# Optimization experiments

Hardware: AMD Instinct MI355X
Metric: run time of the kernel (lower is better)

## Reference

```python
import jax, jax.numpy as jnp
import numpy as np

B, S, D, H = 16, 512, 128, 8  # batch, seq, input_size, num_heads
DH = D * H


def setup_inputs() -> dict:
    key = jax.random.key(0)
    ks = jax.random.split(key, 10)
    s_in = 1.0 / np.sqrt(D)
    s_out = 1.0 / np.sqrt(DH)
    return {
        "input1": jax.random.normal(ks[0], (B, S, D), dtype=jnp.float32),
        "input2": jax.random.normal(ks[1], (B, S, D), dtype=jnp.float32),
        "Wq": jax.random.normal(ks[2], (D, DH), dtype=jnp.float32) * s_in,
        "bq": jax.random.normal(ks[3], (DH,), dtype=jnp.float32) * 0.01,
        "Wk": jax.random.normal(ks[4], (D, DH), dtype=jnp.float32) * s_in,
        "bk": jax.random.normal(ks[5], (DH,), dtype=jnp.float32) * 0.01,
        "Wv": jax.random.normal(ks[6], (D, DH), dtype=jnp.float32) * s_in,
        "bv": jax.random.normal(ks[7], (DH,), dtype=jnp.float32) * 0.01,
        "Wo": jax.random.normal(ks[8], (DH, DH), dtype=jnp.float32) * s_out,
        "bo": jax.random.normal(ks[9], (DH,), dtype=jnp.float32) * 0.01,
    }


def reference(input1, input2, Wq, bq, Wk, bk, Wv, bv, Wo, bo):
    b = input1.shape[0]
    d, dh = Wq.shape
    h = dh // d
    scale = 1.0 / (d ** 0.5)

    def proj(x, W, bias):
        # faithful to torch: view(B, h, -1, d) on a [B, S, h*d] tensor (row-major)
        return (x @ W + bias).reshape(b, h, -1, d)

    def half(xq, xk, xv):
        q = proj(xq, Wq, bq)  # [B,h,S,d]
        k = proj(xk, Wk, bk)
        v = proj(xv, Wv, bv)
        scores = jnp.einsum('bhqd,bhkd->bhqk', q, k) * scale
        attn = jax.nn.softmax(scores, axis=-1)
        # original transposes attention before the value matmul: attn^T @ v
        out = jnp.einsum('bhqk,bhqd->bhkd', attn, v)
        out = out.reshape(b, -1, h * d)
        return out @ Wo + bo

    out1 = half(input1, input2, input1)
    out2 = half(input2, input1, input2)
    return (out1, out2)
```

## Files before the change

kernel.cpp:

```cpp
#include <hip/hip_runtime.h>
#include <cstdint>
#include <cstddef>

using f32x4 = __attribute__((ext_vector_type(4))) float;
using s16x8 = __attribute__((ext_vector_type(8))) short;
typedef uint16_t u16;
typedef uint32_t u32;

__device__ __forceinline__ u16 f2bf(float x) {
  union { float f; u32 u; } v; v.f = x;
  u32 r = v.u + 0x7FFFu + ((v.u >> 16) & 1u);
  return (u16)(r >> 16);
}

__device__ __forceinline__ void async16(void* ldsdst, const void* gsrc) {
  __builtin_amdgcn_global_load_lds(
      (const __attribute__((address_space(1))) u32*)gsrc,
      (__attribute__((address_space(3))) u32*)ldsdst, 16, 0, 0);
}

__global__ void cast_x(const float* __restrict__ in1, const float* __restrict__ in2,
                       u16* __restrict__ X) {
  int i = blockIdx.x * blockDim.x + threadIdx.x;
  const float* src = (i < 262144) ? (in1 + (size_t)i * 4) : (in2 + (size_t)(i - 262144) * 4);
  float4 v = *(const float4*)src;
  u16 o0 = f2bf(v.x), o1 = f2bf(v.y), o2 = f2bf(v.z), o3 = f2bf(v.w);
  u32 w0 = (u32)o0 | ((u32)o1 << 16);
  u32 w1 = (u32)o2 | ((u32)o3 << 16);
  *(uint2*)(X + (size_t)i * 4) = make_uint2(w0, w1);
}

__global__ void transp_w(const float* __restrict__ W, u16* __restrict__ Wt, int R, int C) {
  __shared__ float tile[32][33];
  int bx = blockIdx.x * 32;
  int by = blockIdx.y * 32;
  int tx = threadIdx.x, ty = threadIdx.y;
  #pragma unroll
  for (int i = 0; i < 4; ++i)
    tile[ty + i * 8][tx] = W[(size_t)(by + ty + i * 8) * C + bx + tx];
  __syncthreads();
  #pragma unroll
  for (int i = 0; i < 4; ++i)
    Wt[(size_t)(bx + ty + i * 8) * R + by + tx] = f2bf(tile[tx][ty + i * 8]);
}

template<int KDIM, bool OUTBF16>
__global__ __launch_bounds__(256, 2) void gemm16(
    const u16* __restrict__ A, const u16* __restrict__ Bt,
    const float* __restrict__ bias, void* __restrict__ outp) {
  __shared__ char lds[32768];
  char* Asw = lds;
  char* Bsw = lds + 16384;
  const int t = threadIdx.x;
  const int w = t >> 6, l = t & 63;
  const int l15 = l & 15, lg = l >> 4;
  const int wm = w >> 1, wn = w & 1;
  const size_t m0 = (size_t)blockIdx.x * 128;
  const int n0 = blockIdx.y * 128;

  f32x4 acc[4][4] = {};

  for (int k0 = 0; k0 < KDIM; k0 += 64) {
    #pragma unroll
    for (int p = 0; p < 4; ++p) {
      int idx = p * 256 + t;
      int row = idx >> 3, u = idx & 7;
      const char* sa = (const char*)(A + (m0 + row) * (size_t)KDIM + k0) + ((u ^ (row & 7)) << 4);
      async16(Asw + p * 4096 + w * 1024, sa);
      const char* sb = (const char*)(Bt + (size_t)(n0 + row) * KDIM + k0) + ((u ^ (row & 7)) << 4);
      async16(Bsw + p * 4096 + w * 1024, sb);
    }
    __syncthreads();
    s16x8 af[4][2], bfr[4][2];
    #pragma unroll
    for (int it = 0; it < 4; ++it) {
      int m = wm * 64 + it * 16 + l15;
      int n = wn * 64 + it * 16 + l15;
      #pragma unroll
      for (int st = 0; st < 2; ++st) {
        af[it][st]  = *(const s16x8*)(Asw + m * 128 + ((lg * 16 + st * 64) ^ ((m & 7) << 4)));
        bfr[it][st] = *(const s16x8*)(Bsw + n * 128 + ((lg * 16 + st * 64) ^ ((n & 7) << 4)));
      }
    }
    #pragma unroll
    for (int st = 0; st < 2; ++st)
      #pragma unroll
      for (int mt = 0; mt < 4; ++mt)
        #pragma unroll
        for (int nt = 0; nt < 4; ++nt)
          acc[mt][nt] = __builtin_amdgcn_mfma_f32_16x16x32_bf16(af[mt][st], bfr[nt][st], acc[mt][nt], 0, 0, 0);
    __syncthreads();
  }

  float bv[4];
  #pragma unroll
  for (int nt = 0; nt < 4; ++nt) bv[nt] = bias[n0 + wn * 64 + nt * 16 + l15];
  #pragma unroll
  for (int mt = 0; mt < 4; ++mt) {
    #pragma unroll
    for (int nt = 0; nt < 4; ++nt) {
      size_t ncol = n0 + wn * 64 + nt * 16 + l15;
      #pragma unroll
      for (int r = 0; r < 4; ++r) {
        size_t m = m0 + wm * 64 + mt * 16 + lg * 4 + r;
        float v = acc[mt][nt][r] + bv[nt];
        if constexpr (OUTBF16) ((u16*)outp)[m * 1024 + ncol] = f2bf(v);
        else                   ((float*)outp)[m * 1024 + ncol] = v;
      }
    }
  }
}

__global__ __launch_bounds__(512) void vtrans(const u16* __restrict__ Pv, u16* __restrict__ Vt) {
  __shared__ char lds3[65536];
  const int t = threadIdx.x;
  const int w = t >> 6;
  const int rb = blockIdx.x;
  const size_t inrow = (size_t)rb * 64;
  char* vtb = (char*)(Vt + (size_t)rb * 65536);

  for (int pass = 0; pass < 2; ++pass) {
    #pragma unroll
    for (int p = 0; p < 8; ++p) {
      int idx = p * 512 + t;
      int r = idx >> 7, u = idx & 127;
      const char* src = (const char*)(Pv + (inrow + pass * 32 + r) * 1024) + ((u ^ (r & 31)) << 4);
      async16(lds3 + p * 8192 + w * 1024, src);
    }
    __syncthreads();
    int dd0 = t >> 5, r = t & 31;
    #pragma unroll
    for (int dg = 0; dg < 8; ++dg) {
      int dd = dd0 + dg * 16;
      u16 vals[8];
      #pragma unroll
      for (int cb = 0; cb < 8; ++cb) {
        int off = (cb * 256 + dd * 2) ^ ((r & 31) << 4);
        vals[cb] = *(const u16*)(lds3 + r * 2048 + off);
      }
      uint4 o;
      o.x = (u32)vals[0] | ((u32)vals[1] << 16);
      o.y = (u32)vals[2] | ((u32)vals[3] << 16);
      o.z = (u32)vals[4] | ((u32)vals[5] << 16);
      o.w = (u32)vals[6] | ((u32)vals[7] << 16);
      *(uint4*)(vtb + (size_t)dd * 1024 + (pass * 32 + r) * 16) = o;
    }
    __syncthreads();
  }
}

__global__ __launch_bounds__(512, 2) void attn_kernel(
    const u16* __restrict__ Pq, const u16* __restrict__ Pk,
    const u16* __restrict__ Vt, u16* __restrict__ outp) {
  extern __shared__ char lds[];
  char* Abase = lds + 131072;
  float* scratch = (float*)Abase;

  const int t = threadIdx.x;
  const int w = t >> 6;
  const int l = t & 63;
  const int l15 = l & 15, lg = l >> 4;

  const int wg = blockIdx.x;
  const int half = wg >> 7;
  const int b = (wg >> 3) & 15;
  const int hh = wg & 7;

  const size_t qrow = (size_t)half * 8192 + b * 512 + hh * 64;
  const size_t krow = (size_t)(1 - half) * 8192 + b * 512 + hh * 64;
  const char* vtb = (const char*)(Vt + ((size_t)half * 128 + b * 8 + hh) * 65536);

  #pragma unroll
  for (int p = 0; p < 16; ++p) {
    int idx = p * 512 + t;
    int k = idx >> 4, u = idx & 15;
    const char* src = (const char*)Pk + (krow + (k >> 3)) * 2048
                      + (size_t)((k & 7) * 256 + ((u ^ (k & 7)) << 4));
    async16(lds + p * 8192 + w * 1024, src);
  }
  __syncthreads();

  f32x4 O[4][8] = {};
  const float SCL = 0.127517432f;

  for (int qi = 0; qi < 16; ++qi) {
    const int q0 = qi * 32;
    s16x8 qf[2][4];
    #pragma unroll
    for (int nt = 0; nt < 2; ++nt) {
      int sg = q0 + nt * 16 + l15;
      const char* qp = (const char*)Pq + (qrow + (sg >> 3)) * 2048 + (sg & 7) * 256;
      #pragma unroll
      for (int st = 0; st < 4; ++st)
        qf[nt][st] = *(const s16x8*)(qp + lg * 16 + st * 64);
    }
    f32x4 S0[4] = {}, S1[4] = {};
    #pragma unroll
    for (int mt = 0; mt < 4; ++mt) {
      int k = w * 64 + mt * 16 + l15;
      const char* kp = lds + k * 256;
      int key = (k & 7) << 4;
      #pragma unroll
      for (int st = 0; st < 4; ++st) {
        s16x8 kf = *(const s16x8*)(kp + ((lg * 16 + st * 64) ^ key));
        S0[mt] = __builtin_amdgcn_mfma_f32_16x16x32_bf16(kf, qf[0][st], S0[mt], 0, 0, 0);
        S1[mt] = __builtin_amdgcn_mfma_f32_16x16x32_bf16(kf, qf[1][st], S1[mt], 0, 0, 0);
      }
    }
    float sum0 = 0.f, sum1 = 0.f;
    #pragma unroll
    for (int mt = 0; mt < 4; ++mt)
      #pragma unroll
      for (int r = 0; r < 4; ++r) {
        float e0 = exp2f(S0[mt][r] * SCL); S0[mt][r] = e0; sum0 += e0;
        float e1 = exp2f(S1[mt][r] * SCL); S1[mt][r] = e1; sum1 += e1;
      }
    sum0 += __shfl_xor(sum0, 16); sum0 += __shfl_xor(sum0, 32);
    sum1 += __shfl_xor(sum1, 16); sum1 += __shfl_xor(sum1, 32);
    if (l < 16) { scratch[w * 32 + l] = sum0; scratch[w * 32 + l + 16] = sum1; }
    __syncthreads();
    float L0 = 0.f, L1 = 0.f;
    #pragma unroll
    for (int ww = 0; ww < 8; ++ww) {
      L0 += scratch[ww * 32 + l15];
      L1 += scratch[ww * 32 + 16 + l15];
    }
    float inv0 = 1.0f / L0, inv1 = 1.0f / L1;
    __syncthreads();
    s16x8 vf[8];
    #pragma unroll
    for (int nt = 0; nt < 8; ++nt) {
      int d = nt * 16 + l15;
      vf[nt] = *(const s16x8*)(vtb + (size_t)d * 1024 + (q0 + lg * 8) * 2);
    }
    #pragma unroll
    for (int nt = 0; nt < 2; ++nt) {
      int q = nt * 16 + l15;
      float inv = nt ? inv1 : inv0;
      char* arow = Abase + q * 1024;
      int key = (q & 7) << 4;
      #pragma unroll
      for (int mt = 0; mt < 4; ++mt) {
        float a0 = (nt ? S1[mt][0] : S0[mt][0]) * inv;
        float a1 = (nt ? S1[mt][1] : S0[mt][1]) * inv;
        float a2 = (nt ? S1[mt][2] : S0[mt][2]) * inv;
        float a3 = (nt ? S1[mt][3] : S0[mt][3]) * inv;
        u32 w0 = (u32)f2bf(a0) | ((u32)f2bf(a1) << 16);
        u32 w1 = (u32)f2bf(a2) | ((u32)f2bf(a3) << 16);
        int k0b = (w * 64 + mt * 16 + lg * 4) * 2;
        *(uint2*)(arow + (k0b ^ key)) = make_uint2(w0, w1);
      }
    }
    __syncthreads();
    #pragma unroll
    for (int mt = 0; mt < 4; ++mt) {
      int kb = (w * 64 + mt * 16 + l15) * 2;
      s16x8 af;
      #pragma unroll
      for (int j = 0; j < 8; ++j) {
        int c = lg * 8 + j;
        af[j] = (short)(*(const u16*)(Abase + c * 1024 + (kb ^ (j << 4))));
      }
      #pragma unroll
      for (int nt = 0; nt < 8; ++nt)
        O[mt][nt] = __builtin_amdgcn_mfma_f32_16x16x32_bf16(af, vf[nt], O[mt][nt], 0, 0, 0);
    }
    __syncthreads();
  }

  #pragma unroll
  for (int mt = 0; mt < 4; ++mt)
    #pragma unroll
    for (int nt = 0; nt < 8; ++nt) {
      int d2 = (nt * 16 + l15) * 2;
      #pragma unroll
      for (int r = 0; r < 4; ++r) {
        int k = w * 64 + mt * 16 + lg * 4 + r;
        *(u16*)(lds + k * 256 + (d2 ^ ((k & 7) << 5))) = f2bf(O[mt][nt][r]);
      }
    }
  __syncthreads();
  char* ob = (char*)outp + qrow * 2048;
  #pragma unroll
  for (int p = 0; p < 16; ++p) {
    int g = p * 512 + t;
    int k = g >> 4, u = g & 15;
    uint4 v = *(const uint4*)(lds + k * 256 + ((u * 16) ^ ((k & 7) << 5)));
    *(uint4*)(ob + (size_t)(k >> 3) * 2048 + (k & 7) * 256 + u * 16) = v;
  }
}

extern "C" void kernel_launch(void* const* d_in, const int* in_sizes, int n_in,
                              void* d_out, int out_size, void* d_ws, size_t ws_size,
                              hipStream_t stream) {
  const float* in1 = (const float*)d_in[0];
  const float* in2 = (const float*)d_in[1];
  const float* Wq  = (const float*)d_in[2];
  const float* bq  = (const float*)d_in[3];
  const float* Wk  = (const float*)d_in[4];
  const float* bk  = (const float*)d_in[5];
  const float* Wv  = (const float*)d_in[6];
  const float* bv  = (const float*)d_in[7];
  const float* Wo  = (const float*)d_in[8];
  const float* bo  = (const float*)d_in[9];

  char* ws = (char*)d_ws;
  u16* X    = (u16*)(ws);
  u16* Wtq  = (u16*)(ws + 4194304);
  u16* Wtk  = (u16*)(ws + 4456448);
  u16* Wtv  = (u16*)(ws + 4718592);
  u16* Wto  = (u16*)(ws + 4980736);
  u16* Pq   = (u16*)(ws + 7077888);
  u16* Pk   = (u16*)(ws + 40632320);
  u16* Pv   = (u16*)(ws + 74186752);
  u16* Vt   = (u16*)(ws + 107741184);

  (void)hipFuncSetAttribute((const void*)attn_kernel,
                            hipFuncAttributeMaxDynamicSharedMemorySize, 163840);

  cast_x<<<2048, 256, 0, stream>>>(in1, in2, X);
  transp_w<<<dim3(32, 4),  dim3(32, 8), 0, stream>>>(Wq, Wtq, 128, 1024);
  transp_w<<<dim3(32, 4),  dim3(32, 8), 0, stream>>>(Wk, Wtk, 128, 1024);
  transp_w<<<dim3(32, 4),  dim3(32, 8), 0, stream>>>(Wv, Wtv, 128, 1024);
  transp_w<<<dim3(32, 32), dim3(32, 8), 0, stream>>>(Wo, Wto, 1024, 1024);

  gemm16<128, true><<<dim3(128, 8), 256, 0, stream>>>(X, Wtq, bq, Pq);
  gemm16<128, true><<<dim3(128, 8), 256, 0, stream>>>(X, Wtk, bk, Pk);
  gemm16<128, true><<<dim3(128, 8), 256, 0, stream>>>(X, Wtv, bv, Pv);

  vtrans<<<256, 512, 0, stream>>>(Pv, Vt);

  attn_kernel<<<256, 512, 163840, stream>>>(Pq, Pk, Vt, Pv);

  gemm16<1024, false><<<dim3(128, 8), 256, 0, stream>>>(Pv, Wto, bo, d_out);
}
```

Before: 267.9 us.

## Merge QKV GEMMs and weight transposes; software-pipeline Q loads in attention

The three weight-transpose launches and the three QKV projection GEMMs are each merged into a single launch. This relies on Wtq/Wtk/Wtv and Pq/Pk/Pv sitting contiguously in the workspace, which the offsets confirm. In the attention kernel, the next Q tile is prefetched into double-buffered registers while the current tile is processed. The kernel also adds s_setprio around the MFMA sections, changes the LDS swizzle for the probability tile, and uses packed bf16 conversion. These changes cut launch overhead and hide global Q-load latency, at the cost of more registers and a changed rounding path.

```diff
diff --git a/kernel.cpp b/kernel.cpp
--- a/kernel.cpp
+++ b/kernel.cpp
@@ -1,4 +1,5 @@
 #include <hip/hip_runtime.h>
+#include <hip/hip_bf16.h>
 #include <cstdint>
 #include <cstddef>
 
@@ -42,6 +43,24 @@
   #pragma unroll
   for (int i = 0; i < 4; ++i)
     Wt[(size_t)(bx + ty + i * 8) * R + by + tx] = f2bf(tile[tx][ty + i * 8]);
+}
+
+__global__ void transp_w3(const float* __restrict__ W0, const float* __restrict__ W1,
+                          const float* __restrict__ W2, u16* __restrict__ T0,
+                          u16* __restrict__ T1, u16* __restrict__ T2) {
+  __shared__ float tile[32][33];
+  const float* W = (blockIdx.z == 0) ? W0 : (blockIdx.z == 1) ? W1 : W2;
+  u16*        Wt = (blockIdx.z == 0) ? T0 : (blockIdx.z == 1) ? T1 : T2;
+  int bx = blockIdx.x * 32;
+  int by = blockIdx.y * 32;
+  int tx = threadIdx.x, ty = threadIdx.y;
+  #pragma unroll
+  for (int i = 0; i < 4; ++i)
+    tile[ty + i * 8][tx] = W[(size_t)(by + ty + i * 8) * 1024 + bx + tx];
+  __syncthreads();
+  #pragma unroll
+  for (int i = 0; i < 4; ++i)
+    Wt[(size_t)(bx + ty + i * 8) * 128 + by + tx] = f2bf(tile[tx][ty + i * 8]);
 }
 
 template<int KDIM, bool OUTBF16>
@@ -111,6 +130,74 @@
   }
 }
 
+__global__ __launch_bounds__(256, 2) void gemm_qkv(
+    const u16* __restrict__ A, const u16* __restrict__ Wt3,
+    const float* __restrict__ bq, const float* __restrict__ bk,
+    const float* __restrict__ bvv, u16* __restrict__ P3) {
+  __shared__ char lds[32768];
+  char* Asw = lds;
+  char* Bsw = lds + 16384;
+  const int t = threadIdx.x;
+  const int w = t >> 6, l = t & 63;
+  const int l15 = l & 15, lg = l >> 4;
+  const int wm = w >> 1, wn = w & 1;
+  const size_t m0 = (size_t)blockIdx.x * 128;
+  const int n0 = blockIdx.y * 128;
+
+  f32x4 acc[4][4] = {};
+
+  for (int k0 = 0; k0 < 128; k0 += 64) {
+    #pragma unroll
+    for (int p = 0; p < 4; ++p) {
+      int idx = p * 256 + t;
+      int row = idx >> 3, u = idx & 7;
+      const char* sa = (const char*)(A + (m0 + row) * (size_t)128 + k0) + ((u ^ (row & 7)) << 4);
+      async16(Asw + p * 4096 + w * 1024, sa);
+      const char* sb = (const char*)(Wt3 + (size_t)(n0 + row) * 128 + k0) + ((u ^ (row & 7)) << 4);
+      async16(Bsw + p * 4096 + w * 1024, sb);
+    }
+    __syncthreads();
+    s16x8 af[4][2], bfr[4][2];
+    #pragma unroll
+    for (int it = 0; it < 4; ++it) {
+      int m = wm * 64 + it * 16 + l15;
+      int n = wn * 64 + it * 16 + l15;
+      #pragma unroll
+      for (int st = 0; st < 2; ++st) {
+        af[it][st]  = *(const s16x8*)(Asw + m * 128 + ((lg * 16 + st * 64) ^ ((m & 7) << 4)));
+        bfr[it][st] = *(const s16x8*)(Bsw + n * 128 + ((lg * 16 + st * 64) ^ ((n & 7) << 4)));
+      }
+    }
+    #pragma unroll
+    for (int st = 0; st < 2; ++st)
+      #pragma unroll
+      for (int mt = 0; mt < 4; ++mt)
+        #pragma unroll
+        for (int nt = 0; nt < 4; ++nt)
+          acc[mt][nt] = __builtin_amdgcn_mfma_f32_16x16x32_bf16(af[mt][st], bfr[nt][st], acc[mt][nt], 0, 0, 0);
+    __syncthreads();
+  }
+
+  const int which = n0 >> 10;
+  const float* bias = (which == 0) ? bq : (which == 1) ? bk : bvv;
+  u16* op = P3 + (size_t)which * 16777216;
+  float bv[4];
+  #pragma unroll
+  for (int nt = 0; nt < 4; ++nt) bv[nt] = bias[(n0 + wn * 64 + nt * 16 + l15) & 1023];
+  #pragma unroll
+  for (int mt = 0; mt < 4; ++mt) {
+    #pragma unroll
+    for (int nt = 0; nt < 4; ++nt) {
+      size_t ncol = (n0 + wn * 64 + nt * 16 + l15) & 1023;
+      #pragma unroll
+      for (int r = 0; r < 4; ++r) {
+        size_t m = m0 + wm * 64 + mt * 16 + lg * 4 + r;
+        op[m * 1024 + ncol] = f2bf(acc[mt][nt][r] + bv[nt]);
+      }
+    }
+  }
+}
+
 __global__ __launch_bounds__(512) void vtrans(const u16* __restrict__ Pv, u16* __restrict__ Vt) {
   __shared__ char lds3[65536];
   const int t = threadIdx.x;
@@ -154,7 +241,6 @@
     const u16* __restrict__ Vt, u16* __restrict__ outp) {
   extern __shared__ char lds[];
   char* Abase = lds + 131072;
-  float* scratch = (float*)Abase;
 
   const int t = threadIdx.x;
   const int w = t >> 6;
@@ -178,96 +264,123 @@
                       + (size_t)((k & 7) * 256 + ((u ^ (k & 7)) << 4));
     async16(lds + p * 8192 + w * 1024, src);
   }
+
+  const float SCL = 0.127517432f;
+  s16x8 qfA[2][4], qfB[2][4];
+
+  #pragma unroll
+  for (int nt = 0; nt < 2; ++nt) {
+    int sg = nt * 16 + l15;
+    const char* qp = (const char*)Pq + (qrow + (sg >> 3)) * 2048 + (sg & 7) * 256;
+    #pragma unroll
+    for (int st = 0; st < 4; ++st)
+      qfA[nt][st] = *(const s16x8*)(qp + lg * 16 + st * 64);
+  }
   __syncthreads();
 
   f32x4 O[4][8] = {};
-  const float SCL = 0.127517432f;
-
-  for (int qi = 0; qi < 16; ++qi) {
-    const int q0 = qi * 32;
-    s16x8 qf[2][4];
-    #pragma unroll
-    for (int nt = 0; nt < 2; ++nt) {
-      int sg = q0 + nt * 16 + l15;
-      const char* qp = (const char*)Pq + (qrow + (sg >> 3)) * 2048 + (sg & 7) * 256;
-      #pragma unroll
-      for (int st = 0; st < 4; ++st)
-        qf[nt][st] = *(const s16x8*)(qp + lg * 16 + st * 64);
-    }
-    f32x4 S0[4] = {}, S1[4] = {};
-    #pragma unroll
-    for (int mt = 0; mt < 4; ++mt) {
-      int k = w * 64 + mt * 16 + l15;
-      const char* kp = lds + k * 256;
-      int key = (k & 7) << 4;
-      #pragma unroll
-      for (int st = 0; st < 4; ++st) {
-        s16x8 kf = *(const s16x8*)(kp + ((lg * 16 + st * 64) ^ key));
-        S0[mt] = __builtin_amdgcn_mfma_f32_16x16x32_bf16(kf, qf[0][st], S0[mt], 0, 0, 0);
-        S1[mt] = __builtin_amdgcn_mfma_f32_16x16x32_bf16(kf, qf[1][st], S1[mt], 0, 0, 0);
-      }
-    }
-    float sum0 = 0.f, sum1 = 0.f;
-    #pragma unroll
-    for (int mt = 0; mt < 4; ++mt)
-      #pragma unroll
-      for (int r = 0; r < 4; ++r) {
-        float e0 = exp2f(S0[mt][r] * SCL); S0[mt][r] = e0; sum0 += e0;
-        float e1 = exp2f(S1[mt][r] * SCL); S1[mt][r] = e1; sum1 += e1;
-      }
-    sum0 += __shfl_xor(sum0, 16); sum0 += __shfl_xor(sum0, 32);
-    sum1 += __shfl_xor(sum1, 16); sum1 += __shfl_xor(sum1, 32);
-    if (l < 16) { scratch[w * 32 + l] = sum0; scratch[w * 32 + l + 16] = sum1; }
-    __syncthreads();
-    float L0 = 0.f, L1 = 0.f;
-    #pragma unroll
-    for (int ww = 0; ww < 8; ++ww) {
-      L0 += scratch[ww * 32 + l15];
-      L1 += scratch[ww * 32 + 16 + l15];
-    }
-    float inv0 = 1.0f / L0, inv1 = 1.0f / L1;
-    __syncthreads();
-    s16x8 vf[8];
-    #pragma unroll
-    for (int nt = 0; nt < 8; ++nt) {
-      int d = nt * 16 + l15;
-      vf[nt] = *(const s16x8*)(vtb + (size_t)d * 1024 + (q0 + lg * 8) * 2);
-    }
-    #pragma unroll
-    for (int nt = 0; nt < 2; ++nt) {
-      int q = nt * 16 + l15;
-      float inv = nt ? inv1 : inv0;
-      char* arow = Abase + q * 1024;
-      int key = (q & 7) << 4;
-      #pragma unroll
-      for (int mt = 0; mt < 4; ++mt) {
-        float a0 = (nt ? S1[mt][0] : S0[mt][0]) * inv;
-        float a1 = (nt ? S1[mt][1] : S0[mt][1]) * inv;
-        float a2 = (nt ? S1[mt][2] : S0[mt][2]) * inv;
-        float a3 = (nt ? S1[mt][3] : S0[mt][3]) * inv;
-        u32 w0 = (u32)f2bf(a0) | ((u32)f2bf(a1) << 16);
-        u32 w1 = (u32)f2bf(a2) | ((u32)f2bf(a3) << 16);
-        int k0b = (w * 64 + mt * 16 + lg * 4) * 2;
-        *(uint2*)(arow + (k0b ^ key)) = make_uint2(w0, w1);
-      }
-    }
-    __syncthreads();
-    #pragma unroll
-    for (int mt = 0; mt < 4; ++mt) {
-      int kb = (w * 64 + mt * 16 + l15) * 2;
-      s16x8 af;
-      #pragma unroll
-      for (int j = 0; j < 8; ++j) {
-        int c = lg * 8 + j;
-        af[j] = (short)(*(const u16*)(Abase + c * 1024 + (kb ^ (j << 4))));
-      }
-      #pragma unroll
-      for (int nt = 0; nt < 8; ++nt)
-        O[mt][nt] = __builtin_amdgcn_mfma_f32_16x16x32_bf16(af, vf[nt], O[mt][nt], 0, 0, 0);
-    }
-    __syncthreads();
-  }
-
+  float* slotw = (float*)(Abase + w * 128);
+
+#define ATTN_BODY(QF, QFN, QI)                                                        \
+  do {                                                                                \
+    const int q0 = (QI) * 32;                                                         \
+    f32x4 S0[4] = {}, S1[4] = {};                                                     \
+    __builtin_amdgcn_s_setprio(1);                                                    \
+    _Pragma("unroll")                                                                 \
+    for (int mt = 0; mt < 4; ++mt) {                                                  \
+      int k = w * 64 + mt * 16 + l15;                                                 \
+      const char* kp = lds + k * 256;                                                 \
+      int key = (k & 7) << 4;                                                         \
+      _Pragma("unroll")                                                               \
+      for (int st = 0; st < 4; ++st) {                                                \
+        s16x8 kf = *(const s16x8*)(kp + ((lg * 16 + st * 64) ^ key));                 \
+        S0[mt] = __builtin_amdgcn_mfma_f32_16x16x32_bf16(kf, QF[0][st], S0[mt], 0, 0, 0); \
+        S1[mt] = __builtin_amdgcn_mfma_f32_16x16x32_bf16(kf, QF[1][st], S1[mt], 0, 0, 0); \
+      }                                                                               \
+    }                                                                                 \
+    __builtin_amdgcn_s_setprio(0);                                                    \
+    if ((QI) < 15) {                \
+      _Pragma("unroll")                                                               \
+      for (int nt = 0; nt < 2; ++nt) {                                                \
+        int sg = q0 + 32 + nt * 16 + l15;                                             \
+        const char* qp = (const char*)Pq + (qrow + (sg >> 3)) * 2048 + (sg & 7) * 256;\
+        _Pragma("unroll")                                                             \
+        for (int st = 0; st < 4; ++st)                                                \
+          QFN[nt][st] = *(const s16x8*)(qp + lg * 16 + st * 64);                      \
+      }                                                                               \
+    }                                                                                 \
+    float sum0 = 0.f, sum1 = 0.f;                                                     \
+    _Pragma("unroll")                                                                 \
+    for (int mt = 0; mt < 4; ++mt)                                                    \
+      _Pragma("unroll")                                                               \
+      for (int r = 0; r < 4; ++r) {                                                   \
+        float e0 = exp2f(S0[mt][r] * SCL); S0[mt][r] = e0; sum0 += e0;                \
+        float e1 = exp2f(S1[mt][r] * SCL); S1[mt][r] = e1; sum1 += e1;                \
+      }                                                                               \
+    sum0 += __shfl_xor(sum0, 16); sum0 += __shfl_xor(sum0, 32);                       \
+    sum1 += __shfl_xor(sum1, 16); sum1 += __shfl_xor(sum1, 32);                       \
+    if (l < 16) { slotw[l] = sum0; slotw[16 + l] = sum1; }                            \
+    __syncthreads();                                        \
+    float L0 = 0.f, L1 = 0.f;                                                         \
+    _Pragma("unroll")                                                                 \
+    for (int ww = 0; ww < 8; ++ww) {                                                  \
+      const float* sl = (const float*)(Abase + ww * 128);                             \
+      L0 += sl[l15];                                                                  \
+      L1 += sl[16 + l15];                                                             \
+    }                                                                                 \
+    float inv0 = 1.0f / L0, inv1 = 1.0f / L1;                                         \
+    __syncthreads();                  \
+                 \
+    s16x8 vf[8];                                                                      \
+    _Pragma("unroll")                                                                 \
+    for (int nt = 0; nt < 8; ++nt) {                                                  \
+      int d = nt * 16 + l15;                                                          \
+      vf[nt] = *(const s16x8*)(vtb + (size_t)d * 1024 + (q0 + lg * 8) * 2);           \
+    }                                                                                 \
+     \
+    _Pragma("unroll")                                                                 \
+    for (int nt = 0; nt < 2; ++nt) {                                                  \
+      int q = nt * 16 + l15;                                                          \
+      float inv = nt ? inv1 : inv0;                                                   \
+      int key = ((q & 7) << 4) ^ (((q >> 3) & 3) << 5);                               \
+      char* arow = Abase + q * 1024;                                                  \
+      _Pragma("unroll")                                                               \
+      for (int mt = 0; mt < 4; ++mt) {                                                \
+        f32x4 s = nt ? S1[mt] : S0[mt];                                               \
+        __hip_bfloat162 h01 = __float22bfloat162_rn(make_float2(s[0] * inv, s[1] * inv)); \
+        __hip_bfloat162 h23 = __float22bfloat162_rn(make_float2(s[2] * inv, s[3] * inv)); \
+        uint2 pk; pk.x = *(u32*)&h01; pk.y = *(u32*)&h23;                             \
+        int k0b = (w * 64 + mt * 16 + lg * 4) * 2;                                    \
+        *(uint2*)(arow + (k0b ^ key)) = pk;                                           \
+      }                                                                               \
+    }                                                                                 \
+     \
+    __builtin_amdgcn_s_setprio(1);                                                    \
+    _Pragma("unroll")                                                                 \
+    for (int mt = 0; mt < 4; ++mt) {                                                  \
+      int kb = (w * 64 + mt * 16 + l15) * 2;                                          \
+      s16x8 af;                                                                       \
+      _Pragma("unroll")                                                               \
+      for (int j = 0; j < 8; ++j) {                                                   \
+        int c = lg * 8 + j;                                                           \
+        int key = (j << 4) ^ (lg << 5);                                               \
+        af[j] = (short)(*(const u16*)(Abase + c * 1024 + (kb ^ key)));                \
+      }                                                                               \
+      _Pragma("unroll")                                                               \
+      for (int nt = 0; nt < 8; ++nt)                                                  \
+        O[mt][nt] = __builtin_amdgcn_mfma_f32_16x16x32_bf16(af, vf[nt], O[mt][nt], 0, 0, 0); \
+    }                                                                                 \
+    __builtin_amdgcn_s_setprio(0);                                                    \
+  } while (0)
+
+  #pragma unroll 1
+  for (int qi = 0; qi < 16; qi += 2) {
+    ATTN_BODY(qfA, qfB, qi);
+    ATTN_BODY(qfB, qfA, qi + 1);
+  }
+#undef ATTN_BODY
+
+  __syncthreads();
   #pragma unroll
   for (int mt = 0; mt < 4; ++mt)
     #pragma unroll
@@ -319,14 +432,10 @@
                             hipFuncAttributeMaxDynamicSharedMemorySize, 163840);
 
   cast_x<<<2048, 256, 0, stream>>>(in1, in2, X);
-  transp_w<<<dim3(32, 4),  dim3(32, 8), 0, stream>>>(Wq, Wtq, 128, 1024);
-  transp_w<<<dim3(32, 4),  dim3(32, 8), 0, stream>>>(Wk, Wtk, 128, 1024);
-  transp_w<<<dim3(32, 4),  dim3(32, 8), 0, stream>>>(Wv, Wtv, 128, 1024);
+  transp_w3<<<dim3(32, 4, 3), dim3(32, 8), 0, stream>>>(Wq, Wk, Wv, Wtq, Wtk, Wtv);
   transp_w<<<dim3(32, 32), dim3(32, 8), 0, stream>>>(Wo, Wto, 1024, 1024);
 
-  gemm16<128, true><<<dim3(128, 8), 256, 0, stream>>>(X, Wtq, bq, Pq);
-  gemm16<128, true><<<dim3(128, 8), 256, 0, stream>>>(X, Wtk, bk, Pk);
-  gemm16<128, true><<<dim3(128, 8), 256, 0, stream>>>(X, Wtv, bv, Pv);
+  gemm_qkv<<<dim3(128, 24), 256, 0, stream>>>(X, Wtq, bq, bk, bv, Pq);
 
   vtrans<<<256, 512, 0, stream>>>(Pv, Vt);
 
```

Measured after the change: 423.4 us. 1.58x slower.
